# Kernel tuning notes

Hardware: AMD Instinct MI355X
Metric: run time of the kernel (lower is better)

The kernel has to match this reference:

```python
import jax, jax.numpy as jnp
import numpy as np

B, S, V, H = 16, 256, 32, 256
LN_EPS = 1e-5


def setup_inputs() -> dict:
    key = jax.random.key(0)
    ks = jax.random.split(key, 8)
    sW = 1.0 / np.sqrt(H)
    return {
        "x": jax.random.normal(ks[0], (B, S, V, 1), jnp.float32),
        "W1": jax.random.normal(ks[1], (V, H), jnp.float32),          # linear1: input_size=1
        "b1": jax.random.normal(ks[2], (V, H), jnp.float32) * 0.1,
        "W2": jax.random.normal(ks[3], (V, H, H), jnp.float32) * sW,
        "b2": jax.random.normal(ks[4], (V, H), jnp.float32) * 0.1,
        "Wg": jax.random.normal(ks[5], (V, H, H), jnp.float32) * sW,
        "bg": jax.random.normal(ks[6], (V, H), jnp.float32) * 0.1,
        "gamma": jnp.ones((V, H), jnp.float32),
        "beta": jnp.zeros((V, H), jnp.float32),
        "Wa": jax.random.normal(ks[7], (H,), jnp.float32) * sW,
        "ba": jnp.zeros((1,), jnp.float32),
    }


def reference(x, W1, b1, W2, b2, Wg, bg, gamma, beta, Wa, ba):
    # Batched GRN over all variables at once (replaces the per-var Python loop).
    # x: [B,S,V,1]; linear1 with input_size=1 is a scalar-vector outer product.
    h = jax.nn.relu(x * W1 + b1)                                  # [B,S,V,H]
    h = jnp.einsum('bsvh,vhk->bsvk', h, W2) + b2                  # linear2
    gated = jax.nn.sigmoid(jnp.einsum('bsvh,vhk->bsvk', h, Wg) + bg) * h
    # residual is the raw scalar input (last dim 1), broadcast over H as in torch
    pre = x + gated                                               # [B,S,V,H]
    mu = jnp.mean(pre, axis=-1, keepdims=True)
    var = jnp.mean(jnp.square(pre - mu), axis=-1, keepdims=True)
    var_outputs = (pre - mu) * jax.lax.rsqrt(var + LN_EPS) * gamma + beta
    # softmax attention pooling over variables
    scores = jnp.einsum('bsvh,h->bsv', var_outputs, Wa) + ba[0]   # [B,S,V]
    attn = jax.nn.softmax(scores, axis=-1)[..., None]             # [B,S,V,1]
    vsn_out = jnp.sum(var_outputs * attn, axis=2)                 # [B,S,H]
    return vsn_out, attn
```

## Files before the change

kernel.cpp:

```cpp
#include <hip/hip_runtime.h>
#include <hip/hip_bf16.h>

typedef _Float16 f16;
typedef _Float16 f16x2 __attribute__((ext_vector_type(2)));
typedef _Float16 f16x4 __attribute__((ext_vector_type(4)));
typedef _Float16 f16x8 __attribute__((ext_vector_type(8)));
typedef float f32x4 __attribute__((ext_vector_type(4)));

#define T_TOK 4096
#define V_N 32
#define H_N 256
#define LN_EPS_F 1e-5f

union U4 { f16x4 h; int i[2]; };

__global__ __launch_bounds__(256) void prep_transpose(
    const float* __restrict__ W2, const float* __restrict__ Wg,
    f16* __restrict__ W2t, f16* __restrict__ Wgt)
{
    __shared__ float tile[64][65];
    int bid = blockIdx.x;
    int w = bid >> 9;
    int rem = bid & 511;
    int v = rem >> 4;
    int kt = (rem >> 2) & 3;
    int nt = rem & 3;
    const float* src = w ? Wg : W2;
    f16* dst = w ? Wgt : W2t;
    const float* base = src + ((size_t)v * H_N + (size_t)kt * 64) * H_N + nt * 64;
    int tid = threadIdx.x;
    #pragma unroll
    for (int p = 0; p < 16; ++p) {
        int idx = p * 256 + tid;
        int r = idx >> 6, c = idx & 63;
        tile[r][c] = base[(size_t)r * H_N + c];
    }
    __syncthreads();
    f16* obase = dst + ((size_t)v * H_N + (size_t)nt * 64) * H_N + kt * 64;
    #pragma unroll
    for (int p = 0; p < 16; ++p) {
        int idx = p * 256 + tid;
        int r = idx >> 6, c = idx & 63;
        obase[(size_t)r * H_N + c] = (f16)tile[c][r];
    }
}

__global__ __launch_bounds__(256) void prep_w1(
    const float* __restrict__ W1, const float* __restrict__ b1,
    f16* __restrict__ W1h, f16* __restrict__ b1h)
{
    int i = blockIdx.x * 256 + threadIdx.x;
    W1h[i] = (f16)W1[i];
    b1h[i] = (f16)b1[i];
}

__global__ __launch_bounds__(256, 2) void fused_grn(
    const float* __restrict__ x,
    const f16* __restrict__ W1h, const f16* __restrict__ b1h,
    const f16* __restrict__ W2t, const float* __restrict__ b2,
    const f16* __restrict__ Wgt, const float* __restrict__ bg,
    const float* __restrict__ gamma, const float* __restrict__ beta,
    const float* __restrict__ Wa, const float* __restrict__ ba,
    f16* __restrict__ VO,
    float* __restrict__ scores)
{
    __shared__ f16 H2L[64 * 256];
    __shared__ float sqx[4][4][16][2];
    __shared__ float spx[4][4][16];

    int bid = blockIdx.x;
    int xcd = bid & 7, rr = bid >> 3;
    int v  = (xcd << 2) + (rr >> 6);
    int mt = rr & 63;
    int tid = threadIdx.x;
    int w = tid >> 6, lane = tid & 63;
    int lo = lane & 15, hi = lane >> 4;
    int m0 = mt * 64;

    const f16* W2v = W2t + ((size_t)v << 16);
    const f16* Wgv = Wgt + ((size_t)v << 16);
    const f16* W1v = W1h + (v << 8);
    const f16* b1v = b1h + (v << 8);

    size_t rb0 = (size_t)(w * 64 + lo) * 256 + (hi << 3);

    f16x8 x8[4];
    #pragma unroll
    for (int g = 0; g < 4; ++g) {
        f16 xh = (f16)x[(size_t)(m0 + g * 16 + lo) * V_N + v];
        x8[g] = f16x8{ xh, xh, xh, xh, xh, xh, xh, xh };
    }

    f16x8 afr[2][4];
    f16x8 w8r[2], c8r[2];

    #pragma unroll
    for (int nf = 0; nf < 4; ++nf)
        afr[0][nf] = *(const f16x8*)&W2v[rb0 + (size_t)nf * 4096 + 0 * 32];
    w8r[0] = *(const f16x8*)&W1v[(0 << 5) + (hi << 3)];
    c8r[0] = *(const f16x8*)&b1v[(0 << 5) + (hi << 3)];
    #pragma unroll
    for (int nf = 0; nf < 4; ++nf)
        afr[1][nf] = *(const f16x8*)&W2v[rb0 + (size_t)nf * 4096 + 1 * 32];
    w8r[1] = *(const f16x8*)&W1v[(1 << 5) + (hi << 3)];
    c8r[1] = *(const f16x8*)&b1v[(1 << 5) + (hi << 3)];

    f32x4 acc[4][4] = {};

    #pragma unroll
    for (int s = 0; s < 8; ++s) {
        f16x8 af_[4];
        #pragma unroll
        for (int nf = 0; nf < 4; ++nf) af_[nf] = afr[s & 1][nf];
        f16x8 w8 = w8r[s & 1], c8 = c8r[s & 1];
        if (s < 6) {
            #pragma unroll
            for (int nf = 0; nf < 4; ++nf)
                afr[s & 1][nf] = *(const f16x8*)&W2v[rb0 + (size_t)nf * 4096 + (s + 2) * 32];
            w8r[s & 1] = *(const f16x8*)&W1v[((s + 2) << 5) + (hi << 3)];
            c8r[s & 1] = *(const f16x8*)&b1v[((s + 2) << 5) + (hi << 3)];
        } else {
            #pragma unroll
            for (int nf = 0; nf < 4; ++nf)
                afr[s & 1][nf] = *(const f16x8*)&Wgv[rb0 + (size_t)nf * 4096 + (s - 6) * 32];
        }
        #pragma unroll
        for (int g = 0; g < 4; ++g) {
            f16x8 hv = x8[g] * w8 + c8;
            #pragma unroll
            for (int j = 0; j < 8; ++j) hv[j] = hv[j] > (f16)0 ? hv[j] : (f16)0;
            #pragma unroll
            for (int nf = 0; nf < 4; ++nf)
                acc[g][nf] = __builtin_amdgcn_mfma_f32_16x16x32_f16(
                    af_[nf], hv, acc[g][nf], 0, 0, 0);
        }
    }

    #pragma unroll
    for (int g = 0; g < 4; ++g) {
        int tok = g * 16 + lo;
        #pragma unroll
        for (int nf = 0; nf < 4; ++nf) {
            int n0 = w * 64 + nf * 16 + (hi << 2);
            f32x4 b4 = *(const f32x4*)&b2[(v << 8) + n0];
            f32x4 h = acc[g][nf] + b4;
            U4 u; u.h = f16x4{ (f16)h[0], (f16)h[1], (f16)h[2], (f16)h[3] };
            int gidx = w * 8 + nf * 2 + (hi >> 1);
            int sg = gidx ^ (tok & 31);
            *(f16x4*)&H2L[tok * 256 + sg * 8 + (hi & 1) * 4] = u.h;
            acc[g][nf] = f32x4{ 0.f, 0.f, 0.f, 0.f };
        }
    }
    asm volatile("s_waitcnt lgkmcnt(0)" ::: "memory");
    __builtin_amdgcn_s_barrier();

    #pragma unroll
    for (int s = 0; s < 8; ++s) {
        f16x8 af_[4];
        #pragma unroll
        for (int nf = 0; nf < 4; ++nf) af_[nf] = afr[s & 1][nf];
        if (s < 6) {
            #pragma unroll
            for (int nf = 0; nf < 4; ++nf)
                afr[s & 1][nf] = *(const f16x8*)&Wgv[rb0 + (size_t)nf * 4096 + (s + 2) * 32];
        }
        #pragma unroll
        for (int g = 0; g < 4; ++g) {
            int tok = g * 16 + lo;
            int sg = ((s << 2) + hi) ^ (tok & 31);
            f16x8 bf = *(const f16x8*)&H2L[tok * 256 + sg * 8];
            #pragma unroll
            for (int nf = 0; nf < 4; ++nf)
                acc[g][nf] = __builtin_amdgcn_mfma_f32_16x16x32_f16(
                    af_[nf], bf, acc[g][nf], 0, 0, 0);
        }
    }

    float sr[4] = {}, qr[4] = {};
    #pragma unroll
    for (int g = 0; g < 4; ++g) {
        int tok = g * 16 + lo;
        #pragma unroll
        for (int nf = 0; nf < 4; ++nf) {
            int n0 = w * 64 + nf * 16 + (hi << 2);
            f32x4 bgv = *(const f32x4*)&bg[(v << 8) + n0];
            int gidx = w * 8 + nf * 2 + (hi >> 1);
            int sg = gidx ^ (tok & 31);
            U4 u; u.h = *(const f16x4*)&H2L[tok * 256 + sg * 8 + (hi & 1) * 4];
            #pragma unroll
            for (int r = 0; r < 4; ++r) {
                float a = acc[g][nf][r] + bgv[r];
                float gg = 1.f / (1.f + __expf(-a));
                float val = gg * (float)u.h[r];
                acc[g][nf][r] = val;
                sr[g] += val; qr[g] += val * val;
            }
        }
    }
    #pragma unroll
    for (int g = 0; g < 4; ++g) {
        sr[g] += __shfl_xor(sr[g], 16); sr[g] += __shfl_xor(sr[g], 32);
        qr[g] += __shfl_xor(qr[g], 16); qr[g] += __shfl_xor(qr[g], 32);
    }
    if (hi == 0) {
        #pragma unroll
        for (int g = 0; g < 4; ++g) {
            sqx[w][g][lo][0] = sr[g];
            sqx[w][g][lo][1] = qr[g];
        }
    }
    __syncthreads();
    float mu[4], inv[4];
    #pragma unroll
    for (int g = 0; g < 4; ++g) {
        float st = sqx[0][g][lo][0] + sqx[1][g][lo][0] + sqx[2][g][lo][0] + sqx[3][g][lo][0];
        float qt = sqx[0][g][lo][1] + sqx[1][g][lo][1] + sqx[2][g][lo][1] + sqx[3][g][lo][1];
        mu[g] = st * (1.f / 256.f);
        float var = qt * (1.f / 256.f) - mu[g] * mu[g];
        inv[g] = rsqrtf(var + LN_EPS_F);
    }

    float sp[4] = {};
    #pragma unroll
    for (int g = 0; g < 4; ++g) {
        f16* VOr = VO + ((size_t)v * T_TOK + m0 + g * 16 + lo) * H_N;
        #pragma unroll
        for (int nf = 0; nf < 4; ++nf) {
            int n0 = w * 64 + nf * 16 + (hi << 2);
            f32x4 gm = *(const f32x4*)&gamma[(v << 8) + n0];
            f32x4 bt = *(const f32x4*)&beta[(v << 8) + n0];
            f32x4 wa = *(const f32x4*)&Wa[n0];
            f16x4 ov;
            #pragma unroll
            for (int r = 0; r < 4; ++r) {
                float o = (acc[g][nf][r] - mu[g]) * inv[g] * gm[r] + bt[r];
                sp[g] += o * wa[r];
                ov[r] = (f16)o;
            }
            *(f16x4*)&VOr[n0] = ov;
        }
        sp[g] += __shfl_xor(sp[g], 16); sp[g] += __shfl_xor(sp[g], 32);
    }
    if (hi == 0) {
        #pragma unroll
        for (int g = 0; g < 4; ++g) spx[w][g][lo] = sp[g];
    }
    __syncthreads();
    if (w == 0 && hi == 0) {
        float bav = ba[0];
        #pragma unroll
        for (int g = 0; g < 4; ++g) {
            float t = spx[0][g][lo] + spx[1][g][lo] + spx[2][g][lo] + spx[3][g][lo] + bav;
            scores[(size_t)(m0 + g * 16 + lo) * V_N + v] = t;
        }
    }
}

__global__ __launch_bounds__(128) void pool(
    const f16* __restrict__ VO,
    const float* __restrict__ scores,
    float* __restrict__ out)
{
    int t = blockIdx.x, tid = threadIdx.x;
    __shared__ float sc[V_N];
    if (tid < V_N) sc[tid] = scores[t * V_N + tid];
    __syncthreads();
    float mx = -1e30f;
    #pragma unroll
    for (int v = 0; v < V_N; ++v) mx = fmaxf(mx, sc[v]);
    float e[V_N];
    float sum = 0.f;
    #pragma unroll
    for (int v = 0; v < V_N; ++v) { e[v] = __expf(sc[v] - mx); sum += e[v]; }
    float isum = 1.f / sum;
    float a0 = 0.f, a1 = 0.f;
    #pragma unroll
    for (int v = 0; v < V_N; ++v) {
        f16x2 vv = *(const f16x2*)&VO[((size_t)v * T_TOK + t) * H_N + tid * 2];
        float ww = e[v] * isum;
        a0 = fmaf((float)vv[0], ww, a0);
        a1 = fmaf((float)vv[1], ww, a1);
    }
    *(float2*)&out[(size_t)t * H_N + tid * 2] = make_float2(a0, a1);
    if (tid < V_N)
        out[(size_t)T_TOK * H_N + (size_t)t * V_N + tid] = e[tid] * isum;
}

extern "C" void kernel_launch(void* const* d_in, const int* in_sizes, int n_in,
                              void* d_out, int out_size, void* d_ws, size_t ws_size,
                              hipStream_t stream)
{
    const float* x     = (const float*)d_in[0];
    const float* W1    = (const float*)d_in[1];
    const float* b1    = (const float*)d_in[2];
    const float* W2    = (const float*)d_in[3];
    const float* b2    = (const float*)d_in[4];
    const float* Wg    = (const float*)d_in[5];
    const float* bg    = (const float*)d_in[6];
    const float* gamma = (const float*)d_in[7];
    const float* beta  = (const float*)d_in[8];
    const float* Wa    = (const float*)d_in[9];
    const float* ba    = (const float*)d_in[10];
    float* out = (float*)d_out;

    char* ws = (char*)d_ws;
    f16* W2t = (f16*)ws;
    f16* Wgt = (f16*)(ws + ((size_t)4 << 20));
    f16* VO  = (f16*)(ws + ((size_t)8 << 20));
    float* scores = (float*)(ws + ((size_t)72 << 20));
    f16* W1h = (f16*)(ws + ((size_t)72 << 20) + (512 << 10));
    f16* b1h = (f16*)(ws + ((size_t)72 << 20) + (528 << 10));

    prep_transpose<<<1024, 256, 0, stream>>>(W2, Wg, W2t, Wgt);
    prep_w1<<<32, 256, 0, stream>>>(W1, b1, W1h, b1h);
    fused_grn<<<2048, 256, 0, stream>>>(x, W1h, b1h, W2t, b2, Wgt, bg,
                                        gamma, beta, Wa, ba, VO, scores);
    pool<<<4096, 128, 0, stream>>>(VO, scores, out);
}
```

Baseline: 126.7 us.

## Stage W2 fragments via global_load_lds triple buffer and raise occupancy

The first GEMM now streams W2 tiles into a triple-buffered LDS region with direct global-to-LDS loads, pipelined with vmcnt waits, instead of holding the fragments in registers. The LDS pool is shared with the H2L activation buffer, which gets a new 4-element-granularity XOR swizzle. Launch bounds are raised to 3 blocks per SIMD-group. The intent is to cut register pressure and VMEM latency so more waves are resident. The cost is extra LDS traffic and synchronisation, and a risk that the hand-counted waits do not match the loads actually issued.

```diff
diff --git a/kernel.cpp b/kernel.cpp
--- a/kernel.cpp
+++ b/kernel.cpp
@@ -13,6 +13,12 @@
 #define LN_EPS_F 1e-5f
 
 union U4 { f16x4 h; int i[2]; };
+
+__device__ __forceinline__ void gload16(const f16* g, f16* l) {
+    __builtin_amdgcn_global_load_lds(
+        (const __attribute__((address_space(1))) void*)g,
+        (__attribute__((address_space(3))) void*)l, 16, 0, 0);
+}
 
 __global__ __launch_bounds__(256) void prep_transpose(
     const float* __restrict__ W2, const float* __restrict__ Wg,
@@ -54,7 +60,7 @@
     b1h[i] = (f16)b1[i];
 }
 
-__global__ __launch_bounds__(256, 2) void fused_grn(
+__global__ __launch_bounds__(256, 3) void fused_grn(
     const float* __restrict__ x,
     const f16* __restrict__ W1h, const f16* __restrict__ b1h,
     const f16* __restrict__ W2t, const float* __restrict__ b2,
@@ -64,9 +70,11 @@
     f16* __restrict__ VO,
     float* __restrict__ scores)
 {
-    __shared__ f16 H2L[64 * 256];
-    __shared__ float sqx[4][4][16][2];
-    __shared__ float spx[4][4][16];
+    __shared__ __align__(16) char pool_[52224];
+    f16* Wb  = (f16*)pool_;
+    f16* H2L = (f16*)pool_;
+    float* sqx = (float*)(pool_ + 49152);
+    float* spx = (float*)(pool_ + 49152 + 2048);
 
     int bid = blockIdx.x;
     int xcd = bid & 7, rr = bid >> 3;
@@ -82,7 +90,23 @@
     const f16* W1v = W1h + (v << 8);
     const f16* b1v = b1h + (v << 8);
 
-    size_t rb0 = (size_t)(w * 64 + lo) * 256 + (hi << 3);
+    auto stageg = [&](const f16* Wv, int s, int buf) {
+        int cs = (lane & 3) ^ ((lane >> 2) & 3);
+        #pragma unroll
+        for (int i = 0; i < 4; ++i) {
+            int n = ((w * 4 + i) << 4) + (lane >> 2);
+            gload16(Wv + ((size_t)n << 8) + (s << 5) + (cs << 3),
+                    &Wb[buf * 8192 + ((w * 4 + i) << 9)]);
+        }
+    };
+
+    stageg(W2v, 0, 0);
+    stageg(W2v, 1, 1);
+
+    f16x8 w8A = *(const f16x8*)&W1v[(0 << 5) + (hi << 3)];
+    f16x8 c8A = *(const f16x8*)&b1v[(0 << 5) + (hi << 3)];
+    f16x8 w8B = *(const f16x8*)&W1v[(1 << 5) + (hi << 3)];
+    f16x8 c8B = *(const f16x8*)&b1v[(1 << 5) + (hi << 3)];
 
     f16x8 x8[4];
     #pragma unroll
@@ -91,49 +115,55 @@
         x8[g] = f16x8{ xh, xh, xh, xh, xh, xh, xh, xh };
     }
 
-    f16x8 afr[2][4];
-    f16x8 w8r[2], c8r[2];
-
-    #pragma unroll
-    for (int nf = 0; nf < 4; ++nf)
-        afr[0][nf] = *(const f16x8*)&W2v[rb0 + (size_t)nf * 4096 + 0 * 32];
-    w8r[0] = *(const f16x8*)&W1v[(0 << 5) + (hi << 3)];
-    c8r[0] = *(const f16x8*)&b1v[(0 << 5) + (hi << 3)];
-    #pragma unroll
-    for (int nf = 0; nf < 4; ++nf)
-        afr[1][nf] = *(const f16x8*)&W2v[rb0 + (size_t)nf * 4096 + 1 * 32];
-    w8r[1] = *(const f16x8*)&W1v[(1 << 5) + (hi << 3)];
-    c8r[1] = *(const f16x8*)&b1v[(1 << 5) + (hi << 3)];
-
     f32x4 acc[4][4] = {};
-
-    #pragma unroll
-    for (int s = 0; s < 8; ++s) {
-        f16x8 af_[4];
-        #pragma unroll
-        for (int nf = 0; nf < 4; ++nf) af_[nf] = afr[s & 1][nf];
-        f16x8 w8 = w8r[s & 1], c8 = c8r[s & 1];
-        if (s < 6) {
-            #pragma unroll
-            for (int nf = 0; nf < 4; ++nf)
-                afr[s & 1][nf] = *(const f16x8*)&W2v[rb0 + (size_t)nf * 4096 + (s + 2) * 32];
-            w8r[s & 1] = *(const f16x8*)&W1v[((s + 2) << 5) + (hi << 3)];
-            c8r[s & 1] = *(const f16x8*)&b1v[((s + 2) << 5) + (hi << 3)];
-        } else {
-            #pragma unroll
-            for (int nf = 0; nf < 4; ++nf)
-                afr[s & 1][nf] = *(const f16x8*)&Wgv[rb0 + (size_t)nf * 4096 + (s - 6) * 32];
-        }
-        #pragma unroll
-        for (int g = 0; g < 4; ++g) {
-            f16x8 hv = x8[g] * w8 + c8;
-            #pragma unroll
-            for (int j = 0; j < 8; ++j) hv[j] = hv[j] > (f16)0 ? hv[j] : (f16)0;
-            #pragma unroll
-            for (int nf = 0; nf < 4; ++nf)
-                acc[g][nf] = __builtin_amdgcn_mfma_f32_16x16x32_f16(
-                    af_[nf], hv, acc[g][nf], 0, 0, 0);
-        }
+    const int afbase = ((hi ^ (lo & 3)) << 3);
+    const int rwb = (w * 64 + lo) << 5;
+
+#define WAITV(N) asm volatile("s_waitcnt vmcnt(" #N ")" ::: "memory")
+
+#define G1STEP(W8, C8, S)                                                        \
+    {                                                                            \
+        f16x8 w8_ = W8, c8_ = C8;                                                \
+        if (S < 6) {                                                             \
+            stageg(W2v, S + 2, (S + 2) % 3);                                     \
+            W8 = *(const f16x8*)&W1v[((S + 2) << 5) + (hi << 3)];                \
+            C8 = *(const f16x8*)&b1v[((S + 2) << 5) + (hi << 3)];                \
+        }                                                                        \
+        f16x8 hv_[4];                                                            \
+        _Pragma("unroll")                                                        \
+        for (int g = 0; g < 4; ++g) {                                            \
+            f16x8 t = x8[g] * w8_ + c8_;                                         \
+            _Pragma("unroll")                                                    \
+            for (int j = 0; j < 8; ++j) t[j] = t[j] > (f16)0 ? t[j] : (f16)0;    \
+            hv_[g] = t;                                                          \
+        }                                                                        \
+        _Pragma("unroll")                                                        \
+        for (int nf = 0; nf < 4; ++nf) {                                         \
+            f16x8 af = *(const f16x8*)&Wb[(S % 3) * 8192 + rwb + (nf << 9) + afbase]; \
+            _Pragma("unroll")                                                    \
+            for (int g = 0; g < 4; ++g)                                          \
+                acc[g][nf] = __builtin_amdgcn_mfma_f32_16x16x32_f16(             \
+                    af, hv_[g], acc[g][nf], 0, 0, 0);                            \
+        }                                                                        \
+    }
+
+    WAITV(0);  G1STEP(w8A, c8A, 0)
+               G1STEP(w8B, c8B, 1)
+    WAITV(6);  G1STEP(w8A, c8A, 2)
+    WAITV(6);  G1STEP(w8B, c8B, 3)
+    WAITV(6);  G1STEP(w8A, c8A, 4)
+    WAITV(6);  G1STEP(w8B, c8B, 5)
+    WAITV(6);  G1STEP(w8A, c8A, 6)
+    WAITV(0);  G1STEP(w8B, c8B, 7)
+
+    __syncthreads();
+
+    f16x8 afA[4], afB[4];
+    #pragma unroll
+    for (int nf = 0; nf < 4; ++nf) {
+        size_t rb = (size_t)((w * 64 + nf * 16 + lo) << 8) + (hi << 3);
+        afA[nf] = *(const f16x8*)&Wgv[rb];
+        afB[nf] = *(const f16x8*)&Wgv[rb + 32];
     }
 
     #pragma unroll
@@ -145,36 +175,43 @@
             f32x4 b4 = *(const f32x4*)&b2[(v << 8) + n0];
             f32x4 h = acc[g][nf] + b4;
             U4 u; u.h = f16x4{ (f16)h[0], (f16)h[1], (f16)h[2], (f16)h[3] };
-            int gidx = w * 8 + nf * 2 + (hi >> 1);
-            int sg = gidx ^ (tok & 31);
-            *(f16x4*)&H2L[tok * 256 + sg * 8 + (hi & 1) * 4] = u.h;
+            int gg = w * 16 + nf * 4 + hi;
+            int sg = gg ^ (2 * lo);
+            *(f16x4*)&H2L[tok * 256 + sg * 4] = u.h;
             acc[g][nf] = f32x4{ 0.f, 0.f, 0.f, 0.f };
         }
     }
-    asm volatile("s_waitcnt lgkmcnt(0)" ::: "memory");
-    __builtin_amdgcn_s_barrier();
-
-    #pragma unroll
-    for (int s = 0; s < 8; ++s) {
-        f16x8 af_[4];
-        #pragma unroll
-        for (int nf = 0; nf < 4; ++nf) af_[nf] = afr[s & 1][nf];
-        if (s < 6) {
-            #pragma unroll
-            for (int nf = 0; nf < 4; ++nf)
-                afr[s & 1][nf] = *(const f16x8*)&Wgv[rb0 + (size_t)nf * 4096 + (s + 2) * 32];
-        }
-        #pragma unroll
-        for (int g = 0; g < 4; ++g) {
-            int tok = g * 16 + lo;
-            int sg = ((s << 2) + hi) ^ (tok & 31);
-            f16x8 bf = *(const f16x8*)&H2L[tok * 256 + sg * 8];
-            #pragma unroll
-            for (int nf = 0; nf < 4; ++nf)
-                acc[g][nf] = __builtin_amdgcn_mfma_f32_16x16x32_f16(
-                    af_[nf], bf, acc[g][nf], 0, 0, 0);
-        }
-    }
+    __syncthreads();
+
+#define G2STEP(CUR, S)                                                           \
+    {                                                                            \
+        _Pragma("unroll")                                                        \
+        for (int g = 0; g < 4; ++g) {                                            \
+            int tok = g * 16 + lo;                                               \
+            int sgr = ((S) * 8 + hi * 2) ^ (2 * lo);                             \
+            f16x8 bf = *(const f16x8*)&H2L[tok * 256 + sgr * 4];                 \
+            _Pragma("unroll")                                                    \
+            for (int nf = 0; nf < 4; ++nf)                                       \
+                acc[g][nf] = __builtin_amdgcn_mfma_f32_16x16x32_f16(             \
+                    CUR[nf], bf, acc[g][nf], 0, 0, 0);                           \
+        }                                                                        \
+        if (S < 6) {                                                             \
+            _Pragma("unroll")                                                    \
+            for (int nf = 0; nf < 4; ++nf) {                                     \
+                size_t rb = (size_t)((w * 64 + nf * 16 + lo) << 8) + (hi << 3);  \
+                CUR[nf] = *(const f16x8*)&Wgv[rb + ((S + 2) << 5)];              \
+            }                                                                    \
+        }                                                                        \
+    }
+
+    G2STEP(afA, 0)
+    G2STEP(afB, 1)
+    G2STEP(afA, 2)
+    G2STEP(afB, 3)
+    G2STEP(afA, 4)
+    G2STEP(afB, 5)
+    G2STEP(afA, 6)
+    G2STEP(afB, 7)
 
     float sr[4] = {}, qr[4] = {};
     #pragma unroll
@@ -184,14 +221,14 @@
         for (int nf = 0; nf < 4; ++nf) {
             int n0 = w * 64 + nf * 16 + (hi << 2);
             f32x4 bgv = *(const f32x4*)&bg[(v << 8) + n0];
-            int gidx = w * 8 + nf * 2 + (hi >> 1);
-            int sg = gidx ^ (tok & 31);
-            U4 u; u.h = *(const f16x4*)&H2L[tok * 256 + sg * 8 + (hi & 1) * 4];
+            int gg = w * 16 + nf * 4 + hi;
+            int sg = gg ^ (2 * lo);
+            U4 u; u.h = *(const f16x4*)&H2L[tok * 256 + sg * 4];
             #pragma unroll
             for (int r = 0; r < 4; ++r) {
                 float a = acc[g][nf][r] + bgv[r];
-                float gg = 1.f / (1.f + __expf(-a));
-                float val = gg * (float)u.h[r];
+                float gsig = 1.f / (1.f + __expf(-a));
+                float val = gsig * (float)u.h[r];
                 acc[g][nf][r] = val;
                 sr[g] += val; qr[g] += val * val;
             }
@@ -205,16 +242,20 @@
     if (hi == 0) {
         #pragma unroll
         for (int g = 0; g < 4; ++g) {
-            sqx[w][g][lo][0] = sr[g];
-            sqx[w][g][lo][1] = qr[g];
+            sqx[((w * 4 + g) * 16 + lo) * 2 + 0] = sr[g];
+            sqx[((w * 4 + g) * 16 + lo) * 2 + 1] = qr[g];
         }
     }
     __syncthreads();
     float mu[4], inv[4];
     #pragma unroll
     for (int g = 0; g < 4; ++g) {
-        float st = sqx[0][g][lo][0] + sqx[1][g][lo][0] + sqx[2][g][lo][0] + sqx[3][g][lo][0];
-        float qt = sqx[0][g][lo][1] + sqx[1][g][lo][1] + sqx[2][g][lo][1] + sqx[3][g][lo][1];
+        float st = 0.f, qt = 0.f;
+        #pragma unroll
+        for (int ww = 0; ww < 4; ++ww) {
+            st += sqx[((ww * 4 + g) * 16 + lo) * 2 + 0];
+            qt += sqx[((ww * 4 + g) * 16 + lo) * 2 + 1];
+        }
         mu[g] = st * (1.f / 256.f);
         float var = qt * (1.f / 256.f) - mu[g] * mu[g];
         inv[g] = rsqrtf(var + LN_EPS_F);
@@ -243,17 +284,21 @@
     }
     if (hi == 0) {
         #pragma unroll
-        for (int g = 0; g < 4; ++g) spx[w][g][lo] = sp[g];
+        for (int g = 0; g < 4; ++g) spx[(w * 4 + g) * 16 + lo] = sp[g];
     }
     __syncthreads();
     if (w == 0 && hi == 0) {
         float bav = ba[0];
         #pragma unroll
         for (int g = 0; g < 4; ++g) {
-            float t = spx[0][g][lo] + spx[1][g][lo] + spx[2][g][lo] + spx[3][g][lo] + bav;
+            float t = spx[(0 * 4 + g) * 16 + lo] + spx[(1 * 4 + g) * 16 + lo]
+                    + spx[(2 * 4 + g) * 16 + lo] + spx[(3 * 4 + g) * 16 + lo] + bav;
             scores[(size_t)(m0 + g * 16 + lo) * V_N + v] = t;
         }
     }
+#undef G1STEP
+#undef G2STEP
+#undef WAITV
 }
 
 __global__ __launch_bounds__(128) void pool(
```

After: 111.8 us. 11.8% less time.

## Split fused GRN into two kernels with per-variable weights staged in LDS

Applied to the files above, without the earlier changes.

Replaces the single fused GRN kernel with two kernels. The first computes H2 and writes it to global memory; the second computes the gate, layer norm and scores from the stored H2. Each block stages one variable's full 256x256 fp16 weight matrix in LDS through direct global-to-LDS loads and then processes 512 tokens, so weights are reused across many tokens instead of being re-fetched per 64-token tile. The cost is an extra global round trip for H2 and one more launch. Only 256 blocks of 512 threads run, with 128KB+ of LDS each, which limits occupancy.

```diff
diff --git a/kernel.cpp b/kernel.cpp
--- a/kernel.cpp
+++ b/kernel.cpp
@@ -12,7 +12,16 @@
 #define H_N 256
 #define LN_EPS_F 1e-5f
 
-union U4 { f16x4 h; int i[2]; };
+__device__ __forceinline__ void gload16(const f16* g, f16* l) {
+    __builtin_amdgcn_global_load_lds(
+        (const __attribute__((address_space(1))) void*)g,
+        (__attribute__((address_space(3))) void*)l, 16, 0, 0);
+}
+__device__ __forceinline__ void gload16f(const float* g, float* l) {
+    __builtin_amdgcn_global_load_lds(
+        (const __attribute__((address_space(1))) void*)g,
+        (__attribute__((address_space(3))) void*)l, 16, 0, 0);
+}
 
 __global__ __launch_bounds__(256) void prep_transpose(
     const float* __restrict__ W2, const float* __restrict__ Wg,
@@ -54,204 +63,244 @@
     b1h[i] = (f16)b1[i];
 }
 
-__global__ __launch_bounds__(256, 2) void fused_grn(
+__global__ __launch_bounds__(512) void grn_h2(
     const float* __restrict__ x,
     const f16* __restrict__ W1h, const f16* __restrict__ b1h,
     const f16* __restrict__ W2t, const float* __restrict__ b2,
+    f16* __restrict__ H2g)
+{
+    __shared__ f16 W2L[65536];
+    __shared__ f16 W1L[256], b1L[256];
+    __shared__ float b2L[256];
+
+    int bid = blockIdx.x;
+    int xcd = bid & 7, idx = bid >> 3;
+    int v  = (xcd << 2) + (idx & 3);
+    int t0 = (idx >> 2) * 512;
+    int tid = threadIdx.x;
+    int w = tid >> 6, lane = tid & 63;
+    int lo = lane & 15, hi = lane >> 4;
+    int q = w & 3, th = w >> 2;
+
+    const f16* W2v = W2t + ((size_t)v << 16);
+
+    int cs = (lane & 31) ^ ((w * 2 + (lane >> 5)) & 7);
+    #pragma unroll
+    for (int r = 0; r < 16; ++r)
+        gload16(W2v + ((size_t)(r * 16 + w * 2 + (lane >> 5)) << 8) + (cs << 3),
+                &W2L[(r * 16 + w * 2) << 8]);
+    if (w == 0 && lane < 32) gload16(W1h + (v << 8) + (lane << 3), W1L);
+    if (w == 1 && lane < 32) gload16(b1h + (v << 8) + (lane << 3), b1L);
+    if (w == 2) gload16f(b2 + (v << 8) + (lane << 2), b2L);
+
+    float xs[4][4];
+    #pragma unroll
+    for (int st = 0; st < 4; ++st)
+        #pragma unroll
+        for (int g = 0; g < 4; ++g)
+            xs[st][g] = x[(size_t)(t0 + st * 128 + th * 64 + g * 16 + lo) * V_N + v];
+
+    __syncthreads();
+
+    #pragma unroll
+    for (int st = 0; st < 4; ++st) {
+        int m0 = t0 + st * 128 + th * 64;
+        f16x8 x8[4];
+        #pragma unroll
+        for (int g = 0; g < 4; ++g) {
+            f16 xh = (f16)xs[st][g];
+            x8[g] = f16x8{ xh, xh, xh, xh, xh, xh, xh, xh };
+        }
+        f32x4 acc[4][4] = {};
+        #pragma unroll
+        for (int s = 0; s < 8; ++s) {
+            f16x8 w8 = *(const f16x8*)&W1L[(s << 5) + (hi << 3)];
+            f16x8 c8 = *(const f16x8*)&b1L[(s << 5) + (hi << 3)];
+            f16x8 hv[4];
+            #pragma unroll
+            for (int g = 0; g < 4; ++g) {
+                f16x8 t = x8[g] * w8 + c8;
+                #pragma unroll
+                for (int j = 0; j < 8; ++j) t[j] = t[j] > (f16)0 ? t[j] : (f16)0;
+                hv[g] = t;
+            }
+            #pragma unroll
+            for (int nf = 0; nf < 4; ++nf) {
+                f16x8 af = *(const f16x8*)&W2L[((q * 64 + nf * 16 + lo) << 8)
+                                               + ((((s << 2) + hi) ^ (lo & 7)) << 3)];
+                #pragma unroll
+                for (int g = 0; g < 4; ++g)
+                    acc[g][nf] = __builtin_amdgcn_mfma_f32_16x16x32_f16(
+                        af, hv[g], acc[g][nf], 0, 0, 0);
+            }
+        }
+        #pragma unroll
+        for (int nf = 0; nf < 4; ++nf) {
+            int n0 = q * 64 + nf * 16 + (hi << 2);
+            f32x4 b4 = *(const f32x4*)&b2L[n0];
+            #pragma unroll
+            for (int g = 0; g < 4; ++g) {
+                f32x4 h = acc[g][nf] + b4;
+                f16x4 hh = { (f16)h[0], (f16)h[1], (f16)h[2], (f16)h[3] };
+                *(f16x4*)&H2g[((size_t)v * T_TOK + m0 + g * 16 + lo) * H_N + n0] = hh;
+            }
+        }
+    }
+}
+
+__global__ __launch_bounds__(512) void grn_out(
     const f16* __restrict__ Wgt, const float* __restrict__ bg,
     const float* __restrict__ gamma, const float* __restrict__ beta,
     const float* __restrict__ Wa, const float* __restrict__ ba,
-    f16* __restrict__ VO,
+    const f16* H2g,
+    f16* VOg,
     float* __restrict__ scores)
 {
-    __shared__ f16 H2L[64 * 256];
-    __shared__ float sqx[4][4][16][2];
-    __shared__ float spx[4][4][16];
+    __shared__ f16 WgL[65536];
+    __shared__ float bgL[256], gmL[256], btL[256], waL[256];
+    __shared__ float sqx[4][128][2];
+    __shared__ float spxL[4][128];
 
     int bid = blockIdx.x;
-    int xcd = bid & 7, rr = bid >> 3;
-    int v  = (xcd << 2) + (rr >> 6);
-    int mt = rr & 63;
+    int xcd = bid & 7, idx = bid >> 3;
+    int v  = (xcd << 2) + (idx & 3);
+    int t0 = (idx >> 2) * 512;
     int tid = threadIdx.x;
     int w = tid >> 6, lane = tid & 63;
     int lo = lane & 15, hi = lane >> 4;
-    int m0 = mt * 64;
-
-    const f16* W2v = W2t + ((size_t)v << 16);
+    int q = w & 3, th = w >> 2;
+
     const f16* Wgv = Wgt + ((size_t)v << 16);
-    const f16* W1v = W1h + (v << 8);
-    const f16* b1v = b1h + (v << 8);
-
-    size_t rb0 = (size_t)(w * 64 + lo) * 256 + (hi << 3);
-
-    f16x8 x8[4];
-    #pragma unroll
-    for (int g = 0; g < 4; ++g) {
-        f16 xh = (f16)x[(size_t)(m0 + g * 16 + lo) * V_N + v];
-        x8[g] = f16x8{ xh, xh, xh, xh, xh, xh, xh, xh };
-    }
-
-    f16x8 afr[2][4];
-    f16x8 w8r[2], c8r[2];
-
-    #pragma unroll
-    for (int nf = 0; nf < 4; ++nf)
-        afr[0][nf] = *(const f16x8*)&W2v[rb0 + (size_t)nf * 4096 + 0 * 32];
-    w8r[0] = *(const f16x8*)&W1v[(0 << 5) + (hi << 3)];
-    c8r[0] = *(const f16x8*)&b1v[(0 << 5) + (hi << 3)];
-    #pragma unroll
-    for (int nf = 0; nf < 4; ++nf)
-        afr[1][nf] = *(const f16x8*)&W2v[rb0 + (size_t)nf * 4096 + 1 * 32];
-    w8r[1] = *(const f16x8*)&W1v[(1 << 5) + (hi << 3)];
-    c8r[1] = *(const f16x8*)&b1v[(1 << 5) + (hi << 3)];
-
-    f32x4 acc[4][4] = {};
-
-    #pragma unroll
-    for (int s = 0; s < 8; ++s) {
-        f16x8 af_[4];
-        #pragma unroll
-        for (int nf = 0; nf < 4; ++nf) af_[nf] = afr[s & 1][nf];
-        f16x8 w8 = w8r[s & 1], c8 = c8r[s & 1];
-        if (s < 6) {
-            #pragma unroll
-            for (int nf = 0; nf < 4; ++nf)
-                afr[s & 1][nf] = *(const f16x8*)&W2v[rb0 + (size_t)nf * 4096 + (s + 2) * 32];
-            w8r[s & 1] = *(const f16x8*)&W1v[((s + 2) << 5) + (hi << 3)];
-            c8r[s & 1] = *(const f16x8*)&b1v[((s + 2) << 5) + (hi << 3)];
-        } else {
-            #pragma unroll
-            for (int nf = 0; nf < 4; ++nf)
-                afr[s & 1][nf] = *(const f16x8*)&Wgv[rb0 + (size_t)nf * 4096 + (s - 6) * 32];
-        }
-        #pragma unroll
-        for (int g = 0; g < 4; ++g) {
-            f16x8 hv = x8[g] * w8 + c8;
-            #pragma unroll
-            for (int j = 0; j < 8; ++j) hv[j] = hv[j] > (f16)0 ? hv[j] : (f16)0;
-            #pragma unroll
-            for (int nf = 0; nf < 4; ++nf)
-                acc[g][nf] = __builtin_amdgcn_mfma_f32_16x16x32_f16(
-                    af_[nf], hv, acc[g][nf], 0, 0, 0);
-        }
-    }
-
-    #pragma unroll
-    for (int g = 0; g < 4; ++g) {
-        int tok = g * 16 + lo;
-        #pragma unroll
-        for (int nf = 0; nf < 4; ++nf) {
-            int n0 = w * 64 + nf * 16 + (hi << 2);
-            f32x4 b4 = *(const f32x4*)&b2[(v << 8) + n0];
-            f32x4 h = acc[g][nf] + b4;
-            U4 u; u.h = f16x4{ (f16)h[0], (f16)h[1], (f16)h[2], (f16)h[3] };
-            int gidx = w * 8 + nf * 2 + (hi >> 1);
-            int sg = gidx ^ (tok & 31);
-            *(f16x4*)&H2L[tok * 256 + sg * 8 + (hi & 1) * 4] = u.h;
-            acc[g][nf] = f32x4{ 0.f, 0.f, 0.f, 0.f };
-        }
-    }
-    asm volatile("s_waitcnt lgkmcnt(0)" ::: "memory");
-    __builtin_amdgcn_s_barrier();
-
-    #pragma unroll
-    for (int s = 0; s < 8; ++s) {
-        f16x8 af_[4];
-        #pragma unroll
-        for (int nf = 0; nf < 4; ++nf) af_[nf] = afr[s & 1][nf];
-        if (s < 6) {
-            #pragma unroll
-            for (int nf = 0; nf < 4; ++nf)
-                afr[s & 1][nf] = *(const f16x8*)&Wgv[rb0 + (size_t)nf * 4096 + (s + 2) * 32];
-        }
-        #pragma unroll
-        for (int g = 0; g < 4; ++g) {
-            int tok = g * 16 + lo;
-            int sg = ((s << 2) + hi) ^ (tok & 31);
-            f16x8 bf = *(const f16x8*)&H2L[tok * 256 + sg * 8];
-            #pragma unroll
-            for (int nf = 0; nf < 4; ++nf)
-                acc[g][nf] = __builtin_amdgcn_mfma_f32_16x16x32_f16(
-                    af_[nf], bf, acc[g][nf], 0, 0, 0);
-        }
-    }
-
-    float sr[4] = {}, qr[4] = {};
-    #pragma unroll
-    for (int g = 0; g < 4; ++g) {
-        int tok = g * 16 + lo;
-        #pragma unroll
-        for (int nf = 0; nf < 4; ++nf) {
-            int n0 = w * 64 + nf * 16 + (hi << 2);
-            f32x4 bgv = *(const f32x4*)&bg[(v << 8) + n0];
-            int gidx = w * 8 + nf * 2 + (hi >> 1);
-            int sg = gidx ^ (tok & 31);
-            U4 u; u.h = *(const f16x4*)&H2L[tok * 256 + sg * 8 + (hi & 1) * 4];
-            #pragma unroll
-            for (int r = 0; r < 4; ++r) {
-                float a = acc[g][nf][r] + bgv[r];
-                float gg = 1.f / (1.f + __expf(-a));
-                float val = gg * (float)u.h[r];
-                acc[g][nf][r] = val;
-                sr[g] += val; qr[g] += val * val;
-            }
-        }
-    }
-    #pragma unroll
-    for (int g = 0; g < 4; ++g) {
-        sr[g] += __shfl_xor(sr[g], 16); sr[g] += __shfl_xor(sr[g], 32);
-        qr[g] += __shfl_xor(qr[g], 16); qr[g] += __shfl_xor(qr[g], 32);
-    }
-    if (hi == 0) {
-        #pragma unroll
-        for (int g = 0; g < 4; ++g) {
-            sqx[w][g][lo][0] = sr[g];
-            sqx[w][g][lo][1] = qr[g];
-        }
-    }
+
+    int cs = (lane & 31) ^ ((w * 2 + (lane >> 5)) & 7);
+    #pragma unroll
+    for (int r = 0; r < 16; ++r)
+        gload16(Wgv + ((size_t)(r * 16 + w * 2 + (lane >> 5)) << 8) + (cs << 3),
+                &WgL[(r * 16 + w * 2) << 8]);
+    if (w == 0) gload16f(bg    + (v << 8) + (lane << 2), bgL);
+    if (w == 1) gload16f(gamma + (v << 8) + (lane << 2), gmL);
+    if (w == 2) gload16f(beta  + (v << 8) + (lane << 2), btL);
+    if (w == 3) gload16f(Wa + (lane << 2), waL);
+    float bav = ba[0];
+
     __syncthreads();
-    float mu[4], inv[4];
-    #pragma unroll
-    for (int g = 0; g < 4; ++g) {
-        float st = sqx[0][g][lo][0] + sqx[1][g][lo][0] + sqx[2][g][lo][0] + sqx[3][g][lo][0];
-        float qt = sqx[0][g][lo][1] + sqx[1][g][lo][1] + sqx[2][g][lo][1] + sqx[3][g][lo][1];
-        mu[g] = st * (1.f / 256.f);
-        float var = qt * (1.f / 256.f) - mu[g] * mu[g];
-        inv[g] = rsqrtf(var + LN_EPS_F);
-    }
-
-    float sp[4] = {};
-    #pragma unroll
-    for (int g = 0; g < 4; ++g) {
-        f16* VOr = VO + ((size_t)v * T_TOK + m0 + g * 16 + lo) * H_N;
-        #pragma unroll
-        for (int nf = 0; nf < 4; ++nf) {
-            int n0 = w * 64 + nf * 16 + (hi << 2);
-            f32x4 gm = *(const f32x4*)&gamma[(v << 8) + n0];
-            f32x4 bt = *(const f32x4*)&beta[(v << 8) + n0];
-            f32x4 wa = *(const f32x4*)&Wa[n0];
-            f16x4 ov;
-            #pragma unroll
-            for (int r = 0; r < 4; ++r) {
-                float o = (acc[g][nf][r] - mu[g]) * inv[g] * gm[r] + bt[r];
-                sp[g] += o * wa[r];
-                ov[r] = (f16)o;
-            }
-            *(f16x4*)&VOr[n0] = ov;
-        }
-        sp[g] += __shfl_xor(sp[g], 16); sp[g] += __shfl_xor(sp[g], 32);
-    }
-    if (hi == 0) {
-        #pragma unroll
-        for (int g = 0; g < 4; ++g) spx[w][g][lo] = sp[g];
-    }
-    __syncthreads();
-    if (w == 0 && hi == 0) {
-        float bav = ba[0];
-        #pragma unroll
-        for (int g = 0; g < 4; ++g) {
-            float t = spx[0][g][lo] + spx[1][g][lo] + spx[2][g][lo] + spx[3][g][lo] + bav;
-            scores[(size_t)(m0 + g * 16 + lo) * V_N + v] = t;
+
+    #pragma unroll
+    for (int st = 0; st < 4; ++st) {
+        int m0 = t0 + st * 128 + th * 64;
+        const f16* rp0 = H2g + ((size_t)v * T_TOK + m0 + 0 * 16 + lo) * H_N;
+        const f16* rp1 = H2g + ((size_t)v * T_TOK + m0 + 1 * 16 + lo) * H_N;
+        const f16* rp2 = H2g + ((size_t)v * T_TOK + m0 + 2 * 16 + lo) * H_N;
+        const f16* rp3 = H2g + ((size_t)v * T_TOK + m0 + 3 * 16 + lo) * H_N;
+        const f16* rp[4] = { rp0, rp1, rp2, rp3 };
+        f16* vr0 = VOg + ((size_t)v * T_TOK + m0 + 0 * 16 + lo) * H_N;
+        f16* vr1 = VOg + ((size_t)v * T_TOK + m0 + 1 * 16 + lo) * H_N;
+        f16* vr2 = VOg + ((size_t)v * T_TOK + m0 + 2 * 16 + lo) * H_N;
+        f16* vr3 = VOg + ((size_t)v * T_TOK + m0 + 3 * 16 + lo) * H_N;
+        f16* vr[4] = { vr0, vr1, vr2, vr3 };
+
+        f16x8 bf0[4], bf1[4], bf2[4];
+        #pragma unroll
+        for (int g = 0; g < 4; ++g) {
+            bf0[g] = *(const f16x8*)&rp[g][0 * 32 + (hi << 3)];
+            bf1[g] = *(const f16x8*)&rp[g][1 * 32 + (hi << 3)];
+            bf2[g] = *(const f16x8*)&rp[g][2 * 32 + (hi << 3)];
+        }
+        f32x4 acc[4][4] = {};
+
+#define BSTEP(BF, S)                                                             \
+        {                                                                        \
+            _Pragma("unroll")                                                    \
+            for (int nf = 0; nf < 4; ++nf) {                                     \
+                f16x8 af = *(const f16x8*)&WgL[((q * 64 + nf * 16 + lo) << 8)    \
+                                     + (((((S) << 2) + hi) ^ (lo & 7)) << 3)];   \
+                _Pragma("unroll")                                                \
+                for (int g = 0; g < 4; ++g)                                      \
+                    acc[g][nf] = __builtin_amdgcn_mfma_f32_16x16x32_f16(         \
+                        af, BF[g], acc[g][nf], 0, 0, 0);                         \
+            }                                                                    \
+            if ((S) < 5) {                                                       \
+                _Pragma("unroll")                                                \
+                for (int g = 0; g < 4; ++g)                                      \
+                    BF[g] = *(const f16x8*)&rp[g][((S) + 3) * 32 + (hi << 3)];   \
+            }                                                                    \
+        }
+
+        BSTEP(bf0, 0) BSTEP(bf1, 1) BSTEP(bf2, 2)
+        BSTEP(bf0, 3) BSTEP(bf1, 4) BSTEP(bf2, 5)
+        BSTEP(bf0, 6) BSTEP(bf1, 7)
+#undef BSTEP
+
+        float sr[4] = {}, qr[4] = {};
+        #pragma unroll
+        for (int g = 0; g < 4; ++g) {
+            #pragma unroll
+            for (int nf = 0; nf < 4; ++nf) {
+                int n0 = q * 64 + nf * 16 + (hi << 2);
+                f32x4 bgv = *(const f32x4*)&bgL[n0];
+                f16x4 h2v = *(const f16x4*)&rp[g][n0];
+                #pragma unroll
+                for (int r = 0; r < 4; ++r) {
+                    float a = acc[g][nf][r] + bgv[r];
+                    float sg = 1.f / (1.f + __expf(-a));
+                    float val = sg * (float)h2v[r];
+                    acc[g][nf][r] = val;
+                    sr[g] += val; qr[g] += val * val;
+                }
+            }
+            sr[g] += __shfl_xor(sr[g], 16); sr[g] += __shfl_xor(sr[g], 32);
+            qr[g] += __shfl_xor(qr[g], 16); qr[g] += __shfl_xor(qr[g], 32);
+        }
+        if (hi == 0) {
+            #pragma unroll
+            for (int g = 0; g < 4; ++g) {
+                sqx[q][th * 64 + g * 16 + lo][0] = sr[g];
+                sqx[q][th * 64 + g * 16 + lo][1] = qr[g];
+            }
+        }
+        __syncthreads();
+        float mu[4], inv[4];
+        #pragma unroll
+        for (int g = 0; g < 4; ++g) {
+            int tk = th * 64 + g * 16 + lo;
+            float s_ = sqx[0][tk][0] + sqx[1][tk][0] + sqx[2][tk][0] + sqx[3][tk][0];
+            float q_ = sqx[0][tk][1] + sqx[1][tk][1] + sqx[2][tk][1] + sqx[3][tk][1];
+            mu[g] = s_ * (1.f / 256.f);
+            float var = q_ * (1.f / 256.f) - mu[g] * mu[g];
+            inv[g] = rsqrtf(var + LN_EPS_F);
+        }
+        float sp[4] = {};
+        #pragma unroll
+        for (int g = 0; g < 4; ++g) {
+            #pragma unroll
+            for (int nf = 0; nf < 4; ++nf) {
+                int n0 = q * 64 + nf * 16 + (hi << 2);
+                f32x4 gm = *(const f32x4*)&gmL[n0];
+                f32x4 bt = *(const f32x4*)&btL[n0];
+                f32x4 wa = *(const f32x4*)&waL[n0];
+                f16x4 ov;
+                #pragma unroll
+                for (int r = 0; r < 4; ++r) {
+                    float o = (acc[g][nf][r] - mu[g]) * inv[g] * gm[r] + bt[r];
+                    sp[g] += o * wa[r];
+                    ov[r] = (f16)o;
+                }
+                *(f16x4*)&vr[g][n0] = ov;
+            }
+            sp[g] += __shfl_xor(sp[g], 16); sp[g] += __shfl_xor(sp[g], 32);
+        }
+        if (hi == 0) {
+            #pragma unroll
+            for (int g = 0; g < 4; ++g) spxL[q][th * 64 + g * 16 + lo] = sp[g];
+        }
+        __syncthreads();
+        if (q == 0 && hi == 0) {
+            #pragma unroll
+            for (int g = 0; g < 4; ++g) {
+                int tk = th * 64 + g * 16 + lo;
+                scores[(size_t)(t0 + st * 128 + tk) * V_N + v] =
+                    spxL[0][tk] + spxL[1][tk] + spxL[2][tk] + spxL[3][tk] + bav;
+            }
         }
     }
 }
@@ -306,14 +355,16 @@
     char* ws = (char*)d_ws;
     f16* W2t = (f16*)ws;
     f16* Wgt = (f16*)(ws + ((size_t)4 << 20));
-    f16* VO  = (f16*)(ws + ((size_t)8 << 20));
+    f16* H2g = (f16*)(ws + ((size_t)8 << 20));
     float* scores = (float*)(ws + ((size_t)72 << 20));
     f16* W1h = (f16*)(ws + ((size_t)72 << 20) + (512 << 10));
     f16* b1h = (f16*)(ws + ((size_t)72 << 20) + (528 << 10));
+    const size_t NEED = ((size_t)137 << 20);
+    f16* VOg = (ws_size >= NEED) ? (f16*)(ws + ((size_t)73 << 20)) : H2g;
 
     prep_transpose<<<1024, 256, 0, stream>>>(W2, Wg, W2t, Wgt);
     prep_w1<<<32, 256, 0, stream>>>(W1, b1, W1h, b1h);
-    fused_grn<<<2048, 256, 0, stream>>>(x, W1h, b1h, W2t, b2, Wgt, bg,
-                                        gamma, beta, Wa, ba, VO, scores);
-    pool<<<4096, 128, 0, stream>>>(VO, scores, out);
-}
+    grn_h2<<<256, 512, 0, stream>>>(x, W1h, b1h, W2t, b2, H2g);
+    grn_out<<<256, 512, 0, stream>>>(Wgt, bg, gamma, beta, Wa, ba, H2g, VOg, scores);
+    pool<<<4096, 128, 0, stream>>>(VOg, scores, out);
+}
```

Measured after the change: 127.2 us. No clear change (+0.3%).
